# Kernel optimization log

Hardware: AMD Instinct MI355X
Metric: run time of the kernel (lower is better)

Reference implementation:

```python
import jax, jax.numpy as jnp
import numpy as np


def table_operator(A, B):
    # A, B: (size, batch). Returns (16, size, batch) of soft logic-gate outputs.
    AB = A * B
    A_or_B = A + B - AB
    A_xor_B = A + B - 2.0 * AB
    return jnp.stack([
        jnp.zeros_like(A),          # 0: FALSE
        AB,                         # 1: A AND B
        A - AB,                     # 2: A AND NOT B
        A,                          # 3: A
        B - AB,                     # 4: NOT A AND B
        B,                          # 5: B
        A_xor_B,                    # 6: A XOR B
        A_or_B,                     # 7: A OR B
        1.0 - A_or_B,               # 8: NOR
        1.0 - A_xor_B,              # 9: XNOR
        1.0 - B,                    # 10: NOT B
        1.0 - B + AB,               # 11: B -> A
        1.0 - A,                    # 12: NOT A
        1.0 - A + AB,               # 13: A -> B
        1.0 - AB,                   # 14: NAND
        jnp.ones_like(A),           # 15: TRUE
    ], axis=0)


def setup_inputs() -> dict:
    key = jax.random.key(0)
    k1, k2, k3, k4 = jax.random.split(key, 4)
    prev_size, size, batch = 1024, 1024, 16384
    return {
        "prev_layer_output": jax.random.uniform(k1, (prev_size, batch), jnp.float32),
        "input_A_weights": jax.random.normal(k2, (size, prev_size), jnp.float32),
        "input_B_weights": jax.random.normal(k3, (size, prev_size), jnp.float32),
        "table_weights": jax.random.normal(k4, (16, size), jnp.float32),
    }


def reference(prev_layer_output, input_A_weights, input_B_weights, table_weights):
    # Inference path (torch.is_grad_enabled() == False, drop_out_rate == 0):
    # plain softmaxes, no multiplier shift, no dropout. GradFactor is identity in fwd.
    pA = jax.nn.softmax(input_A_weights, axis=1)   # (size, prev_size)
    pB = jax.nn.softmax(input_B_weights, axis=1)
    pT = jax.nn.softmax(table_weights, axis=0)     # (16, size)
    a = pA @ prev_layer_output                     # (size, batch)
    b = pB @ prev_layer_output                     # (size, batch)
    gates = table_operator(a, b)                   # (16, size, batch)
    return jnp.sum(gates * pT[:, :, None], axis=0)  # (size, batch)
```

## Files before the change

### kernel.cpp

```cpp
#include <hip/hip_runtime.h>
#include <hip/hip_bf16.h>


typedef __attribute__((ext_vector_type(8))) short bf16x8;
typedef __attribute__((ext_vector_type(4))) float f32x4;

__device__ __forceinline__ void gload_lds16(const void* g, void* l) {
    __builtin_amdgcn_global_load_lds(
        (const __attribute__((address_space(1))) void*)g,
        (__attribute__((address_space(3))) void*)l, 16, 0, 0);
}

__global__ __launch_bounds__(256) void softmax_rows_bf16(
    const float* __restrict__ WA, const float* __restrict__ WB,
    __hip_bfloat16* __restrict__ PA, __hip_bfloat16* __restrict__ PB,
    int rows, int cols)
{
    const int b = blockIdx.x;
    const float* W;
    __hip_bfloat16* P;
    if (b < rows) { W = WA + (size_t)b * cols;          P = PA + (size_t)b * cols; }
    else          { W = WB + (size_t)(b - rows) * cols; P = PB + (size_t)(b - rows) * cols; }

    const int t = threadIdx.x;
    const int wave = t >> 6, lane = t & 63;

    float4 v = *(const float4*)&W[t * 4];
    float mx = fmaxf(fmaxf(v.x, v.y), fmaxf(v.z, v.w));
    #pragma unroll
    for (int off = 32; off; off >>= 1) mx = fmaxf(mx, __shfl_xor(mx, off));

    __shared__ float redmax[4];
    __shared__ float redsum[4];
    if (lane == 0) redmax[wave] = mx;
    __syncthreads();
    mx = fmaxf(fmaxf(redmax[0], redmax[1]), fmaxf(redmax[2], redmax[3]));

    float e0 = __expf(v.x - mx), e1 = __expf(v.y - mx);
    float e2 = __expf(v.z - mx), e3 = __expf(v.w - mx);
    float s = e0 + e1 + e2 + e3;
    #pragma unroll
    for (int off = 32; off; off >>= 1) s += __shfl_xor(s, off);
    if (lane == 0) redsum[wave] = s;
    __syncthreads();
    s = redsum[0] + redsum[1] + redsum[2] + redsum[3];

    const float inv = 1.0f / s;
    __align__(8) __hip_bfloat16 o[4];
    o[0] = __float2bfloat16(e0 * inv);
    o[1] = __float2bfloat16(e1 * inv);
    o[2] = __float2bfloat16(e2 * inv);
    o[3] = __float2bfloat16(e3 * inv);
    *(uint2*)&P[t * 4] = *(const uint2*)o;
}

__global__ void table_coef(const float* __restrict__ TW, float4* __restrict__ coef, int size)
{
    const int s = blockIdx.x * blockDim.x + threadIdx.x;
    if (s >= size) return;
    float p[16];
    float mx = -1e30f;
    #pragma unroll
    for (int g = 0; g < 16; ++g) { p[g] = TW[g * size + s]; mx = fmaxf(mx, p[g]); }
    float sum = 0.f;
    #pragma unroll
    for (int g = 0; g < 16; ++g) { p[g] = __expf(p[g] - mx); sum += p[g]; }
    const float inv = 1.0f / sum;
    #pragma unroll
    for (int g = 0; g < 16; ++g) p[g] *= inv;

    float w0  = p[8] + p[9] + p[10] + p[11] + p[12] + p[13] + p[14] + p[15];
    float wA  = p[2] + p[3] + p[6] + p[7] - p[8] - p[9] - p[12] - p[13];
    float wB  = p[4] + p[5] + p[6] + p[7] - p[8] - p[9] - p[10] - p[11];
    float wAB = p[1] - p[2] - p[4] - 2.f * p[6] - p[7]
              + p[8] + 2.f * p[9] + p[11] + p[13] - p[14];
    coef[s] = make_float4(w0, wA, wB, wAB);
}

__global__ __launch_bounds__(256) void transpose_bf16(
    const float* __restrict__ prev, __hip_bfloat16* __restrict__ prevT,
    int K, int N)
{
    __shared__ float ls[64][65];
    const int k0 = blockIdx.y * 64, n0 = blockIdx.x * 64;
    const int t = threadIdx.x;

    {
        const int kr = t >> 4, nc = (t & 15) * 4;
        #pragma unroll
        for (int i = 0; i < 4; ++i) {
            const int k = i * 16 + kr;
            float4 v = *(const float4*)&prev[(size_t)(k0 + k) * N + n0 + nc];
            ls[k][nc + 0] = v.x; ls[k][nc + 1] = v.y;
            ls[k][nc + 2] = v.z; ls[k][nc + 3] = v.w;
        }
    }
    __syncthreads();
    {
        const int n = t >> 2, kc = (t & 3) * 16;
        __align__(16) __hip_bfloat16 tmp[16];
        #pragma unroll
        for (int j = 0; j < 16; ++j) tmp[j] = __float2bfloat16(ls[kc + j][n]);
        __hip_bfloat16* dst = &prevT[(size_t)(n0 + n) * K + k0 + kc];
        *(uint4*)(dst + 0) = *(const uint4*)&tmp[0];
        *(uint4*)(dst + 8) = *(const uint4*)&tmp[8];
    }
}

constexpr int BK_   = 32;
constexpr int NTIL  = 32;
constexpr int BUF   = 32768;
constexpr int BOFF_ = 16384;
constexpr int Kd    = 1024;
constexpr int Nd    = 16384;

__global__ __launch_bounds__(512, 2) void dual_gemm8(
    const __hip_bfloat16* __restrict__ pA,
    const __hip_bfloat16* __restrict__ pB,
    const __hip_bfloat16* __restrict__ prevT,
    const float4* __restrict__ coef,
    float* __restrict__ out)
{
    __shared__ __align__(16) char smem[131072];

    const int t = threadIdx.x;
    const int wave = t >> 6, lane = t & 63;
    const int wr = wave >> 2, wc = wave & 3;
    const int m0 = blockIdx.y * 128;
    const int n0 = blockIdx.x * 256;

    const int fr  = lane & 15;
    const int kg  = lane >> 4;
    const int csw = ((kg ^ ((fr >> 1) & 3)) << 4);
    const int aoff = (wr * 128 + fr) * 64 + csw;
    const int boff = BOFF_ + (wc * 64 + fr) * 64 + csw;

    const int srow = lane >> 2;
    const int sksw = ((lane & 3) ^ ((lane >> 3) & 3)) * 8;
    const int arow = 16 * wave + srow;
    const __hip_bfloat16* gA0 = pA    + (size_t)(m0 + arow) * Kd + sksw;
    const __hip_bfloat16* gA1 = pB    + (size_t)(m0 + arow) * Kd + sksw;
    const __hip_bfloat16* gB0 = prevT + (size_t)(n0 + arow) * Kd + sksw;
    const __hip_bfloat16* gB1 = prevT + (size_t)(n0 + 128 + arow) * Kd + sksw;

    auto STAGE_A = [&](int T) {
        char* base = smem + (T & 3) * BUF + wave * 1024;
        const int kT = T * BK_;
        gload_lds16(gA0 + kT, base);
        gload_lds16(gA1 + kT, base + 8192);
    };
    auto STAGE_B = [&](int T) {
        char* base = smem + (T & 3) * BUF + BOFF_ + wave * 1024;
        const int kT = T * BK_;
        gload_lds16(gB0 + kT, base);
        gload_lds16(gB1 + kT, base + 8192);
    };

    f32x4 acc[8][4] = {};
    bf16x8 af[8], bf_[4];

#define PH_MFMA(I0)                                                         \
    asm volatile("s_waitcnt lgkmcnt(0)" ::: "memory");                      \
    __builtin_amdgcn_sched_barrier(0);                                      \
    __builtin_amdgcn_s_setprio(1);                                          \
    _Pragma("unroll")                                                       \
    for (int i = (I0); i < (I0) + 4; ++i) {                                 \
        _Pragma("unroll")                                                   \
        for (int j = 0; j < 4; ++j)                                         \
            acc[i][j] = __builtin_amdgcn_mfma_f32_16x16x32_bf16(            \
                af[i], bf_[j], acc[i][j], 0, 0, 0);                         \
    }                                                                       \
    __builtin_amdgcn_s_setprio(0);

#define DO_TILE(TT, STG, VMSTR)                                             \
  {                                                                         \
    const char* buf = smem + ((TT) & 3) * BUF;                              \
    _Pragma("unroll")                                                       \
    for (int i = 0; i < 4; ++i)                                             \
        af[i] = *(const bf16x8*)(buf + aoff + i * 1024);                    \
    _Pragma("unroll")                                                       \
    for (int j = 0; j < 4; ++j)                                             \
        bf_[j] = *(const bf16x8*)(buf + boff + j * 1024);                   \
    if (STG) STAGE_A((TT) + 3);                                             \
    __builtin_amdgcn_s_barrier();                                           \
    PH_MFMA(0)                                                              \
    __builtin_amdgcn_s_barrier();                                           \
    _Pragma("unroll")                                                       \
    for (int i = 4; i < 8; ++i)                                             \
        af[i] = *(const bf16x8*)(buf + aoff + i * 1024);                    \
    if (STG) STAGE_B((TT) + 3);                                             \
    asm volatile("s_waitcnt " VMSTR ::: "memory");                          \
    __builtin_amdgcn_s_barrier();                                           \
    PH_MFMA(4)                                                              \
    __builtin_amdgcn_s_barrier();                                           \
  }

    STAGE_A(0); STAGE_B(0);
    STAGE_A(1); STAGE_B(1);
    STAGE_A(2); STAGE_B(2);
    asm volatile("s_waitcnt vmcnt(8)" ::: "memory");
    __builtin_amdgcn_s_barrier();

    for (int tt = 0; tt < NTIL - 3; ++tt) {
        DO_TILE(tt, 1, "vmcnt(8)")
    }
    DO_TILE(NTIL - 3, 0, "vmcnt(4)")
    DO_TILE(NTIL - 2, 0, "vmcnt(0)")
    DO_TILE(NTIL - 1, 0, "vmcnt(0)")

#undef DO_TILE
#undef PH_MFMA

    __syncthreads();
    if (wr == 1) {
        #pragma unroll
        for (int i = 0; i < 8; ++i) {
            #pragma unroll
            for (int j = 0; j < 4; ++j) {
                const int off = ((((wc * 8 + i) * 4 + j) * 64) + lane) * 16;
                *(f32x4*)(smem + off) = acc[i][j];
            }
        }
    }
    __syncthreads();
    if (wr == 0) {
        const int hi = lane >> 4;
        #pragma unroll
        for (int i = 0; i < 8; ++i) {
            float4 cc[4];
            #pragma unroll
            for (int r = 0; r < 4; ++r) cc[r] = coef[m0 + i * 16 + hi * 4 + r];
            #pragma unroll
            for (int j = 0; j < 4; ++j) {
                const f32x4 bb = *(const f32x4*)(smem + ((((wc * 8 + i) * 4 + j) * 64) + lane) * 16);
                const int n = n0 + wc * 64 + j * 16 + fr;
                #pragma unroll
                for (int r = 0; r < 4; ++r) {
                    const int m = m0 + i * 16 + hi * 4 + r;
                    const float a = acc[i][j][r];
                    out[(size_t)m * Nd + n] = cc[r].x + cc[r].y * a + cc[r].z * bb[r]
                                            + cc[r].w * (a * bb[r]);
                }
            }
        }
    }
}

extern "C" void kernel_launch(void* const* d_in, const int* in_sizes, int n_in,
                              void* d_out, int out_size, void* d_ws, size_t ws_size,
                              hipStream_t stream)
{
    const float* prev = (const float*)d_in[0];
    const float* WA   = (const float*)d_in[1];
    const float* WB   = (const float*)d_in[2];
    const float* TW   = (const float*)d_in[3];
    float* out = (float*)d_out;

    const int size      = in_sizes[3] / 16;
    const int prev_size = in_sizes[1] / size;
    const int batch     = in_sizes[0] / prev_size;

    char* ws = (char*)d_ws;
    __hip_bfloat16* prevT = (__hip_bfloat16*)ws;
    size_t off = (size_t)batch * prev_size * sizeof(__hip_bfloat16);
    __hip_bfloat16* pA = (__hip_bfloat16*)(ws + off);
    off += (size_t)size * prev_size * sizeof(__hip_bfloat16);
    __hip_bfloat16* pB = (__hip_bfloat16*)(ws + off);
    off += (size_t)size * prev_size * sizeof(__hip_bfloat16);
    float4* coef = (float4*)(ws + off);

    softmax_rows_bf16<<<dim3(2 * size), dim3(256), 0, stream>>>(
        WA, WB, pA, pB, size, prev_size);
    table_coef<<<dim3((size + 255) / 256), dim3(256), 0, stream>>>(TW, coef, size);
    transpose_bf16<<<dim3(batch / 64, prev_size / 64), dim3(256), 0, stream>>>(
        prev, prevT, prev_size, batch);
    dual_gemm8<<<dim3(batch / 256, size / 128), dim3(512), 0, stream>>>(
        pA, pB, prevT, coef, out);
}
```

Before: 95.44 us.

## Prefetch next K-tile LDS fragments into double-buffered registers during MFMA

Restructures the GEMM main loop so the A-rows-0..3 and B fragments for the next K tile are read from LDS into ping-pong registers while the second half of the current tile's MFMAs runs. This cuts the per-tile barriers from four to one and overlaps LDS reads with matrix math. The cost is extra VGPRs for the duplicated B fragments, plus a loop hardcoded to 32 tiles (28 + 4 unrolled), which ties the code to K=1024. The partial lgkmcnt waits depend on the order in which the LDS loads are issued.

```diff
diff --git a/kernel.cpp b/kernel.cpp
--- a/kernel.cpp
+++ b/kernel.cpp
@@ -157,42 +157,74 @@
     };
 
     f32x4 acc[8][4] = {};
-    bf16x8 af[8], bf_[4];
-
-#define PH_MFMA(I0)                                                         \
+    bf16x8 a03[4], a47[4], bf0[4], bf1[4];
+
+#define DO_TILE(TT, STG, VMSTR, BCUR, BNXT)                                 \
+  {                                                                         \
+    const char* buf  = smem + ((TT) & 3) * BUF;                             \
+    const char* nbuf = smem + (((TT) + 1) & 3) * BUF;                       \
+    _Pragma("unroll")                                                       \
+    for (int i = 0; i < 4; ++i)                                             \
+        a47[i] = *(const bf16x8*)(buf + aoff + (4 + i) * 1024);             \
+    asm volatile("s_waitcnt lgkmcnt(4)" ::: "memory");                      \
+    __builtin_amdgcn_sched_barrier(0);                                      \
+    __builtin_amdgcn_s_setprio(1);                                          \
+    _Pragma("unroll")                                                       \
+    for (int i = 0; i < 4; ++i) {                                           \
+      _Pragma("unroll")                                                     \
+      for (int j = 0; j < 4; ++j)                                           \
+        acc[i][j] = __builtin_amdgcn_mfma_f32_16x16x32_bf16(                \
+            a03[i], BCUR[j], acc[i][j], 0, 0, 0);                           \
+    }                                                                       \
+    __builtin_amdgcn_s_setprio(0);                                          \
+    if (STG) { STAGE_A((TT) + 3); STAGE_B((TT) + 3); }                      \
+    asm volatile("s_waitcnt " VMSTR ::: "memory");                          \
+    __builtin_amdgcn_s_barrier();                                           \
+    _Pragma("unroll")                                                       \
+    for (int i = 0; i < 4; ++i)                                             \
+        a03[i] = *(const bf16x8*)(nbuf + aoff + i * 1024);                  \
+    _Pragma("unroll")                                                       \
+    for (int j = 0; j < 4; ++j)                                             \
+        BNXT[j] = *(const bf16x8*)(nbuf + boff + j * 1024);                 \
+    asm volatile("s_waitcnt lgkmcnt(8)" ::: "memory");                      \
+    __builtin_amdgcn_sched_barrier(0);                                      \
+    __builtin_amdgcn_s_setprio(1);                                          \
+    _Pragma("unroll")                                                       \
+    for (int i = 0; i < 4; ++i) {                                           \
+      _Pragma("unroll")                                                     \
+      for (int j = 0; j < 4; ++j)                                           \
+        acc[4 + i][j] = __builtin_amdgcn_mfma_f32_16x16x32_bf16(            \
+            a47[i], BCUR[j], acc[4 + i][j], 0, 0, 0);                       \
+    }                                                                       \
+    __builtin_amdgcn_s_setprio(0);                                          \
+  }
+
+#define DO_LAST(BCUR)                                                       \
+  {                                                                         \
+    const char* buf = smem + ((NTIL - 1) & 3) * BUF;                        \
+    _Pragma("unroll")                                                       \
+    for (int i = 0; i < 4; ++i)                                             \
+        a47[i] = *(const bf16x8*)(buf + aoff + (4 + i) * 1024);             \
+    asm volatile("s_waitcnt lgkmcnt(4)" ::: "memory");                      \
+    __builtin_amdgcn_sched_barrier(0);                                      \
+    __builtin_amdgcn_s_setprio(1);                                          \
+    _Pragma("unroll")                                                       \
+    for (int i = 0; i < 4; ++i) {                                           \
+      _Pragma("unroll")                                                     \
+      for (int j = 0; j < 4; ++j)                                           \
+        acc[i][j] = __builtin_amdgcn_mfma_f32_16x16x32_bf16(                \
+            a03[i], BCUR[j], acc[i][j], 0, 0, 0);                           \
+    }                                                                       \
     asm volatile("s_waitcnt lgkmcnt(0)" ::: "memory");                      \
     __builtin_amdgcn_sched_barrier(0);                                      \
-    __builtin_amdgcn_s_setprio(1);                                          \
-    _Pragma("unroll")                                                       \
-    for (int i = (I0); i < (I0) + 4; ++i) {                                 \
-        _Pragma("unroll")                                                   \
-        for (int j = 0; j < 4; ++j)                                         \
-            acc[i][j] = __builtin_amdgcn_mfma_f32_16x16x32_bf16(            \
-                af[i], bf_[j], acc[i][j], 0, 0, 0);                         \
+    _Pragma("unroll")                                                       \
+    for (int i = 0; i < 4; ++i) {                                           \
+      _Pragma("unroll")                                                     \
+      for (int j = 0; j < 4; ++j)                                           \
+        acc[4 + i][j] = __builtin_amdgcn_mfma_f32_16x16x32_bf16(            \
+            a47[i], BCUR[j], acc[4 + i][j], 0, 0, 0);                       \
     }                                                                       \
-    __builtin_amdgcn_s_setprio(0);
-
-#define DO_TILE(TT, STG, VMSTR)                                             \
-  {                                                                         \
-    const char* buf = smem + ((TT) & 3) * BUF;                              \
-    _Pragma("unroll")                                                       \
-    for (int i = 0; i < 4; ++i)                                             \
-        af[i] = *(const bf16x8*)(buf + aoff + i * 1024);                    \
-    _Pragma("unroll")                                                       \
-    for (int j = 0; j < 4; ++j)                                             \
-        bf_[j] = *(const bf16x8*)(buf + boff + j * 1024);                   \
-    if (STG) STAGE_A((TT) + 3);                                             \
-    __builtin_amdgcn_s_barrier();                                           \
-    PH_MFMA(0)                                                              \
-    __builtin_amdgcn_s_barrier();                                           \
-    _Pragma("unroll")                                                       \
-    for (int i = 4; i < 8; ++i)                                             \
-        af[i] = *(const bf16x8*)(buf + aoff + i * 1024);                    \
-    if (STG) STAGE_B((TT) + 3);                                             \
-    asm volatile("s_waitcnt " VMSTR ::: "memory");                          \
-    __builtin_amdgcn_s_barrier();                                           \
-    PH_MFMA(4)                                                              \
-    __builtin_amdgcn_s_barrier();                                           \
+    __builtin_amdgcn_s_setprio(0);                                          \
   }
 
     STAGE_A(0); STAGE_B(0);
@@ -200,16 +232,24 @@
     STAGE_A(2); STAGE_B(2);
     asm volatile("s_waitcnt vmcnt(8)" ::: "memory");
     __builtin_amdgcn_s_barrier();
-
-    for (int tt = 0; tt < NTIL - 3; ++tt) {
-        DO_TILE(tt, 1, "vmcnt(8)")
-    }
-    DO_TILE(NTIL - 3, 0, "vmcnt(4)")
-    DO_TILE(NTIL - 2, 0, "vmcnt(0)")
-    DO_TILE(NTIL - 1, 0, "vmcnt(0)")
+    #pragma unroll
+    for (int i = 0; i < 4; ++i)
+        a03[i] = *(const bf16x8*)(smem + aoff + i * 1024);
+    #pragma unroll
+    for (int j = 0; j < 4; ++j)
+        bf0[j] = *(const bf16x8*)(smem + boff + j * 1024);
+
+    for (int tt = 0; tt < 28; tt += 2) {
+        DO_TILE(tt,     1, "vmcnt(8)", bf0, bf1)
+        DO_TILE(tt + 1, 1, "vmcnt(8)", bf1, bf0)
+    }
+    DO_TILE(28, 1, "vmcnt(8)", bf0, bf1)
+    DO_TILE(29, 0, "vmcnt(4)", bf1, bf0)
+    DO_TILE(30, 0, "vmcnt(0)", bf0, bf1)
+    DO_LAST(bf1)
 
 #undef DO_TILE
-#undef PH_MFMA
+#undef DO_LAST
 
     __syncthreads();
     if (wr == 1) {
```

Measured after the change: 93.45 us. 1.02x faster.
